# Kernel tuning notes

Measured on AMD Instinct MI355X. Metric: run time of the kernel, lower is better.

Reference implementation:

```python
import jax, jax.numpy as jnp
import numpy as np

N_P, N_V, N_C, N_A = 8000, 3000, 1500, 6000
CLS = N_C
D = 128
E = 150000
N_TOT = N_P + N_V + N_C + N_A
LAMBDA1 = 1.0


def _cal_matrix(A):
    # row-normalize, leaving all-zero rows untouched (matches cal_matrix)
    d = jnp.sum(A, axis=1)
    safe = jnp.where(d > 0, d, 1.0)
    return jnp.where((d > 0)[:, None], A / safe[:, None], A)


def _linear(x, W, b):
    return x @ W.T + b


def _gru(x, h, Wih, Whh, bih, bhh):
    # torch.nn.GRUCell semantics; gate order r, z, n
    gi = x @ Wih.T + bih
    gh = h @ Whh.T + bhh
    ir, iz, inn = jnp.split(gi, 3, axis=1)
    hr, hz, hn = jnp.split(gh, 3, axis=1)
    r = jax.nn.sigmoid(ir + hr)
    z = jax.nn.sigmoid(iz + hz)
    n = jnp.tanh(inn + r * hn)
    return (1.0 - z) * n + z * h


def _ce_soft(pred, label):
    # torch CrossEntropyLoss with probabilistic targets; NOTE: pred is already
    # softmaxed in the original, so log_softmax is applied on top (faithful double softmax)
    return -jnp.mean(jnp.sum(label * jax.nn.log_softmax(pred, axis=1), axis=1))


def _fuse(e0, e1, W2, b2, W3, b3):
    # attention fusion: leaky_relu(., 0) == relu; softmax over the NODE axis (faithful)
    a = jnp.concatenate([_linear(e0, W2, b2), _linear(e1, W3, b3)], axis=0)  # [2N,1]
    alpha = jax.nn.softmax(jax.nn.relu(a).reshape(2, -1, 1), axis=1)
    return jax.nn.relu(jnp.sum(alpha * jnp.stack([e0, e1], axis=0), axis=0))


def _forward(feat_P, feat_V, feat_C, feat_A, W1, b1, W2, b2, W3, b3,
             L00W, L00b, L01W, L01b, L10W, L10b, L11W, L11b, L12W, L12b,
             g0_Wih, g0_Whh, g0_bih, g0_bhh, g1_Wih, g1_Whh, g1_bih, g1_bhh,
             rel_emb, adj00, adj01, adj10, adj11, adj12, clsA, clsP, clsV, u_s, u_d):
    # self embeddings via shared linear1
    self_P = _linear(feat_P, W1, b1)
    self_V = _linear(feat_V, W1, b1)
    self_C = _linear(feat_C, W1, b1)
    self_A = _linear(feat_A, W1, b1)
    loss_tcp = jnp.float32(0.0)
    # ---- meta-path 0: V -> P -> A (GRUCell 0) ----
    pred = jax.nn.softmax(_linear(feat_V, L00W, L00b), axis=1)        # [N_V, CLS]
    loss_tcp += _ce_soft(pred, clsV)
    tcp = jnp.sum(pred * clsV, axis=1, keepdims=True)                 # bmm([N,1,C],[N,C,1])
    h = adj00 @ (tcp * feat_V)                                        # [N_P, D]
    state_P0 = _gru(feat_P, h, g0_Wih, g0_Whh, g0_bih, g0_bhh)
    pred = jax.nn.softmax(_linear(state_P0, L01W, L01b), axis=1)
    loss_tcp += _ce_soft(pred, clsP)
    tcp = jnp.sum(pred * clsP, axis=1, keepdims=True)
    h = adj01 @ (tcp * state_P0)                                      # [N_A, D]
    state_A0 = _gru(feat_A, h, g0_Wih, g0_Whh, g0_bih, g0_bhh)
    # ---- meta-path 1: A -> P -> V -> C (GRUCell 1) ----
    pred = jax.nn.softmax(_linear(feat_A, L10W, L10b), axis=1)
    loss_tcp += _ce_soft(pred, clsA)
    tcp = jnp.sum(pred * clsA, axis=1, keepdims=True)
    h = adj10 @ (tcp * feat_A)                                        # [N_P, D]
    state_P1 = _gru(feat_P, h, g1_Wih, g1_Whh, g1_bih, g1_bhh)        # appended 3rd, unused by fusion
    pred = jax.nn.softmax(_linear(state_P1, L11W, L11b), axis=1)
    loss_tcp += _ce_soft(pred, clsP)
    tcp = jnp.sum(pred * clsP, axis=1, keepdims=True)
    h = adj11 @ (tcp * state_P1)                                      # [N_V, D]
    state_V1 = _gru(feat_V, h, g1_Wih, g1_Whh, g1_bih, g1_bhh)
    pred = jax.nn.softmax(_linear(state_V1, L12W, L12b), axis=1)
    loss_tcp += _ce_soft(pred, clsV)
    tcp = jnp.sum(pred * clsV, axis=1, keepdims=True)
    h = adj12 @ (tcp * state_V1)                                      # [N_C, D]
    state_C1 = _gru(feat_C, h, g1_Wih, g1_Whh, g1_bih, g1_bhh)
    # ---- attention fusion of (self_emb, first GRU state) per node type ----
    emb_P = _fuse(self_P, state_P0, W2, b2, W3, b3)
    emb_V = _fuse(self_V, state_V1, W2, b2, W3, b3)
    emb_C = _fuse(self_C, state_C1, W2, b2, W3, b3)
    emb_A = _fuse(self_A, state_A0, W2, b2, W3, b3)
    final_ent = jnp.concatenate([emb_P, emb_V, emb_C, emb_A], axis=0)  # order P,V,C,A
    # ---- link scoring ----
    lab_d = u_d[:, 2].astype(jnp.float32)
    lab_s = u_s[:, 2].astype(jnp.float32)
    M_r = rel_emb[u_d[:, 3]]
    inner_d = jnp.sum(M_r * jnp.tanh(final_ent[u_d[:, 0]] + final_ent[u_d[:, 1]]), axis=1)
    inner_s = jnp.sum(final_ent[u_s[:, 0]] * final_ent[u_s[:, 1]], axis=1)
    base = -jnp.sum(jax.nn.log_sigmoid(lab_d * inner_d)) - jnp.sum(jax.nn.log_sigmoid(lab_s * inner_s))
    # l2_loss_emb is 0 in the original; l2_loss is computed but never added to loss_emb
    loss = base + LAMBDA1 * loss_tcp
    return loss, final_ent, rel_emb


def setup_inputs():
    key = jax.random.key(0)
    ki = iter(jax.random.split(key, 48))
    def nk():
        return next(ki)
    def xav(o, i):  # xavier_normal_
        return jax.random.normal(nk(), (o, i), jnp.float32) * jnp.sqrt(2.0 / (o + i))
    def uni(shape):  # torch GRUCell default init
        k = 1.0 / float(np.sqrt(D))
        return jax.random.uniform(nk(), shape, jnp.float32, -k, k)
    def radj(o, i, p=0.003):  # raw binary adjacency
        return (jax.random.uniform(nk(), (o, i)) < p).astype(jnp.float32)

    feat_P = jax.random.normal(nk(), (N_P, D), jnp.float32)
    feat_V = jax.random.normal(nk(), (N_V, D), jnp.float32)
    feat_C = jax.random.normal(nk(), (N_C, D), jnp.float32)
    feat_A = jax.random.normal(nk(), (N_A, D), jnp.float32)
    A00 = radj(N_P, N_V); A01 = radj(N_A, N_P)
    A10 = radj(N_P, N_A); A11 = radj(N_V, N_P); A12 = radj(N_C, N_V)

    inp = dict(
        feat_P=feat_P, feat_V=feat_V, feat_C=feat_C, feat_A=feat_A,
        W1=xav(D, D), b1=jnp.zeros((D,), jnp.float32),
        W2=xav(1, D), b2=jnp.zeros((1,), jnp.float32),
        W3=xav(1, D), b3=jnp.zeros((1,), jnp.float32),
        L00W=xav(CLS, D), L00b=jnp.zeros((CLS,), jnp.float32),
        L01W=xav(CLS, D), L01b=jnp.zeros((CLS,), jnp.float32),
        L10W=xav(CLS, D), L10b=jnp.zeros((CLS,), jnp.float32),
        L11W=xav(CLS, D), L11b=jnp.zeros((CLS,), jnp.float32),
        L12W=xav(CLS, D), L12b=jnp.zeros((CLS,), jnp.float32),
        g0_Wih=uni((3 * D, D)), g0_Whh=uni((3 * D, D)), g0_bih=uni((3 * D,)), g0_bhh=uni((3 * D,)),
        g1_Wih=uni((3 * D, D)), g1_Whh=uni((3 * D, D)), g1_bih=uni((3 * D,)), g1_bhh=uni((3 * D,)),
        rel_emb=jax.random.normal(nk(), (12, D), jnp.float32),
        adj00=_cal_matrix(A00), adj01=_cal_matrix(A01),
        adj10=_cal_matrix(A10), adj11=_cal_matrix(A11), adj12=_cal_matrix(A12),
        clsA=_cal_matrix((A12 @ (A11 @ A10)).T),   # [N_A, CLS]
        clsP=_cal_matrix((A12 @ A11).T),           # [N_P, CLS]
        clsV=_cal_matrix(A12.T),                   # [N_V, CLS]
    )

    def edges(n_cols):
        i = jax.random.randint(nk(), (E,), 0, N_TOT)
        j = jax.random.randint(nk(), (E,), 0, N_TOT)
        lab = jax.random.randint(nk(), (E,), 0, 2) * 2 - 1  # labels in {-1,+1}
        cols = [i, j, lab]
        if n_cols == 4:
            cols.append(jax.random.randint(nk(), (E,), 0, 12))
        return jnp.stack(cols, axis=1)

    inp['u_s'] = edges(3)
    inp['u_d'] = edges(4)
    return inp


def reference(feat_P, feat_V, feat_C, feat_A, W1, b1, W2, b2, W3, b3,
              L00W, L00b, L01W, L01b, L10W, L10b, L11W, L11b, L12W, L12b,
              g0_Wih, g0_Whh, g0_bih, g0_bhh, g1_Wih, g1_Whh, g1_bih, g1_bhh,
              rel_emb, adj00, adj01, adj10, adj11, adj12, clsA, clsP, clsV, u_s, u_d):
    return _forward(feat_P, feat_V, feat_C, feat_A, W1, b1, W2, b2, W3, b3,
                    L00W, L00b, L01W, L01b, L10W, L10b, L11W, L11b, L12W, L12b,
                    g0_Wih, g0_Whh, g0_bih, g0_bhh, g1_Wih, g1_Whh, g1_bih, g1_bhh,
                    rel_emb, adj00, adj01, adj10, adj11, adj12, clsA, clsP, clsV, u_s, u_d)
```

## Files before the change

kernel.cpp:

```cpp
#include <hip/hip_runtime.h>
#include <cstdint>
#include <cstddef>

#define DEV_INLINE __device__ __forceinline__

typedef __attribute__((ext_vector_type(8))) short bf16x8;
typedef __attribute__((ext_vector_type(16))) float f32x16;
struct __align__(8) US4 { unsigned short u[4]; };

DEV_INLINE unsigned short f2bf(float x) {
  unsigned u = __float_as_uint(x);
  return (unsigned short)((u + 0x7FFFu + ((u >> 16) & 1u)) >> 16);
}
DEV_INLINE float bf2f(unsigned short u) { return __uint_as_float(((unsigned)u) << 16); }
DEV_INLINE float2 bfpair(unsigned v) {
  return make_float2(__uint_as_float(v << 16), __uint_as_float(v & 0xFFFF0000u));
}
DEV_INLINE float ftanh(float x) {
  float e = __expf(2.0f * x);
  return 1.0f - 2.0f / (e + 1.0f);
}
DEV_INLINE float softplus_neg(float x) {
  return (x >= 0.f) ? log1pf(__expf(-x)) : (-x + log1pf(__expf(x)));
}

struct CvtSeg { const float* src; unsigned short* dst; int n; int nblk; };
struct CvtArgs { CvtSeg seg[16]; int nseg; };

__global__ __launch_bounds__(256) void convert_bf16_many(CvtArgs args) {
  int b = blockIdx.x;
  int s = 0;
  while (s < args.nseg && b >= args.seg[s].nblk) { b -= args.seg[s].nblk; ++s; }
  if (s >= args.nseg) return;
  int base = b * 1024 + threadIdx.x * 4;
  if (base >= args.seg[s].n) return;
  float4 v = *reinterpret_cast<const float4*>(args.seg[s].src + base);
  US4 o;
  o.u[0] = f2bf(v.x); o.u[1] = f2bf(v.y); o.u[2] = f2bf(v.z); o.u[3] = f2bf(v.w);
  *reinterpret_cast<US4*>(args.seg[s].dst + base) = o;
}

struct GSeg { const unsigned short* X; const unsigned short* W; const float* bias;
              float* C; unsigned short* Cb; int N; int O; int blk0; int xblk; };
struct GSegs { GSeg s[8]; int nseg; };

__global__ __launch_bounds__(256) void gemm_bf16_gseg(GSegs gs) {
  __shared__ __align__(16) unsigned short Xs[128 * 128];
  __shared__ __align__(16) unsigned short Ws[64 * 128];
  int bx = blockIdx.x;
  int si = 0;
  while (si + 1 < gs.nseg && bx >= gs.s[si + 1].blk0) ++si;
  const GSeg& g = gs.s[si];
  int b = bx - g.blk0;
  int bm = (b % g.xblk) * 128;
  int bn = (b / g.xblk) * 64;
  const int tid = threadIdx.x;

#pragma unroll
  for (int i = 0; i < 8; ++i) {
    int s = tid + 256 * i;
    int row = s >> 4, c16 = s & 15;
    uint4 v = make_uint4(0, 0, 0, 0);
    int gr = bm + row;
    if (gr < g.N) v = *reinterpret_cast<const uint4*>(g.X + (size_t)gr * 128 + c16 * 8);
    *reinterpret_cast<uint4*>(&Xs[(row * 16 + (c16 ^ (row & 7))) * 8]) = v;
  }
#pragma unroll
  for (int i = 0; i < 4; ++i) {
    int s = tid + 256 * i;
    int row = s >> 4, c16 = s & 15;
    uint4 v = make_uint4(0, 0, 0, 0);
    int gw = bn + row;
    if (gw < g.O) v = *reinterpret_cast<const uint4*>(g.W + (size_t)gw * 128 + c16 * 8);
    *reinterpret_cast<uint4*>(&Ws[(row * 16 + (c16 ^ (row & 7))) * 8]) = v;
  }
  __syncthreads();

  const int wave = tid >> 6, lane = tid & 63;
  const int l31 = lane & 31, lhi = lane >> 5;

  f32x16 acc0, acc1;
#pragma unroll
  for (int i = 0; i < 16; ++i) { acc0[i] = 0.f; acc1[i] = 0.f; }
  const int ar = wave * 32 + l31;
#pragma unroll
  for (int ks = 0; ks < 8; ++ks) {
    int c16 = ks * 2 + lhi;
    bf16x8 a  = *reinterpret_cast<const bf16x8*>(&Xs[(ar * 16 + (c16 ^ (ar & 7))) * 8]);
    bf16x8 b0 = *reinterpret_cast<const bf16x8*>(&Ws[(l31 * 16 + (c16 ^ (l31 & 7))) * 8]);
    int br1 = 32 + l31;
    bf16x8 b1 = *reinterpret_cast<const bf16x8*>(&Ws[(br1 * 16 + (c16 ^ (br1 & 7))) * 8]);
    acc0 = __builtin_amdgcn_mfma_f32_32x32x16_bf16(a, b0, acc0, 0, 0, 0);
    acc1 = __builtin_amdgcn_mfma_f32_32x32x16_bf16(a, b1, acc1, 0, 0, 0);
  }

  if (g.Cb) {
#pragma unroll
    for (int reg = 0; reg < 16; ++reg) {
      int r = bm + wave * 32 + (reg & 3) + 8 * (reg >> 2) + 4 * lhi;
      if (r < g.N) {
        int c0 = bn + l31;
        if (c0 < g.O) g.Cb[(size_t)r * g.O + c0] = f2bf(acc0[reg] + g.bias[c0]);
        int c1 = bn + 32 + l31;
        if (c1 < g.O) g.Cb[(size_t)r * g.O + c1] = f2bf(acc1[reg] + g.bias[c1]);
      }
    }
  } else {
#pragma unroll
    for (int reg = 0; reg < 16; ++reg) {
      int r = bm + wave * 32 + (reg & 3) + 8 * (reg >> 2) + 4 * lhi;
      if (r < g.N) {
        int c0 = bn + l31;
        if (c0 < g.O) g.C[(size_t)r * g.O + c0] = acc0[reg] + g.bias[c0];
        int c1 = bn + 32 + l31;
        if (c1 < g.O) g.C[(size_t)r * g.O + c1] = acc1[reg] + g.bias[c1];
      }
    }
  }
}

DEV_INLINE void spmv_body_b(const float* __restrict__ A, const float* __restrict__ Xs,
                            unsigned short* __restrict__ Hb, int row, int K,
                            float (*red)[128])
{
  int tid = threadIdx.x, wave = tid >> 6, lane = tid & 63;
  const float4* Arow = reinterpret_cast<const float4*>(A + (size_t)row * K);
  int K4 = K >> 2;
  float acc0 = 0.f, acc1 = 0.f;
  int base = wave * 64;
  int q = base + lane;
  float4 a = (base < K4 && q < K4) ? Arow[q] : make_float4(0.f, 0.f, 0.f, 0.f);
  for (; base < K4; base += 256) {
    int nb = base + 256;
    int nq = nb + lane;
    float4 an = (nb < K4 && nq < K4) ? Arow[nq] : make_float4(0.f, 0.f, 0.f, 0.f);
#pragma unroll
    for (int c = 0; c < 4; ++c) {
      float av = (c == 0) ? a.x : (c == 1) ? a.y : (c == 2) ? a.z : a.w;
      unsigned long long mm = __ballot(av != 0.f);
      while (mm) {
        int b = __builtin_ctzll(mm);
        mm &= mm - 1;
        float v = __shfl(av, b);
        int jj = (base + b) * 4 + c;
        const float* xr = Xs + (size_t)jj * 128;
        acc0 += v * xr[lane];
        acc1 += v * xr[lane + 64];
      }
    }
    a = an;
  }
  red[wave][lane] = acc0;
  red[wave][lane + 64] = acc1;
  __syncthreads();
  if (wave == 0) {
    float r0 = red[0][lane] + red[1][lane] + red[2][lane] + red[3][lane];
    float r1 = red[0][lane + 64] + red[1][lane + 64] + red[2][lane + 64] + red[3][lane + 64];
    Hb[(size_t)row * 128 + lane] = f2bf(r0);
    Hb[(size_t)row * 128 + 64 + lane] = f2bf(r1);
  }
}

__global__ __launch_bounds__(256) void spmv_scan(
    const float* __restrict__ A, const float* __restrict__ Xs,
    unsigned short* __restrict__ Hb, int M, int K)
{
  __shared__ float red[4][128];
  spmv_body_b(A, Xs, Hb, blockIdx.x, K, red);
}

__global__ __launch_bounds__(256) void spmv_scan2(
    const float* __restrict__ A0, const float* __restrict__ X0,
    unsigned short* __restrict__ H0b, int M0, int K0,
    const float* __restrict__ A1, const float* __restrict__ X1,
    unsigned short* __restrict__ H1b, int K1)
{
  __shared__ float red[4][128];
  if ((int)blockIdx.x < M0) spmv_body_b(A0, X0, H0b, blockIdx.x, K0, red);
  else                      spmv_body_b(A1, X1, H1b, blockIdx.x - M0, K1, red);
}

DEV_INLINE void ghgru_body_b(
    const unsigned short* __restrict__ Hb, const unsigned short* __restrict__ Whhb,
    const float* __restrict__ bhh, const unsigned short* __restrict__ gi,
    float* __restrict__ out, unsigned short* __restrict__ outb,
    int M, int bm, unsigned short* As)
{
  const int tid = threadIdx.x;
#pragma unroll
  for (int i = 0; i < 2; ++i) {
    int s = tid + 256 * i;
    int row = s >> 4, c16 = s & 15;
    uint4 v = make_uint4(0, 0, 0, 0);
    int gr = bm + row;
    if (gr < M) v = *reinterpret_cast<const uint4*>(Hb + (size_t)gr * 128 + c16 * 8);
    *reinterpret_cast<uint4*>(&As[(row * 16 + (c16 ^ (row & 7))) * 8]) = v;
  }
  __syncthreads();

  const int wave = tid >> 6, lane = tid & 63;
  const int l31 = lane & 31, lhi = lane >> 5;
  const int d = wave * 32 + l31;

  f32x16 ar, az, an;
#pragma unroll
  for (int i = 0; i < 16; ++i) { ar[i] = 0.f; az[i] = 0.f; an[i] = 0.f; }

#pragma unroll
  for (int ks = 0; ks < 8; ++ks) {
    int c16 = ks * 2 + lhi;
    bf16x8 a = *reinterpret_cast<const bf16x8*>(&As[(l31 * 16 + (c16 ^ (l31 & 7))) * 8]);
    const unsigned short* wb = Whhb + (size_t)c16 * 8;
    bf16x8 br = *reinterpret_cast<const bf16x8*>(wb + (size_t)d * 128);
    bf16x8 bz = *reinterpret_cast<const bf16x8*>(wb + (size_t)(128 + d) * 128);
    bf16x8 bn = *reinterpret_cast<const bf16x8*>(wb + (size_t)(256 + d) * 128);
    ar = __builtin_amdgcn_mfma_f32_32x32x16_bf16(a, br, ar, 0, 0, 0);
    az = __builtin_amdgcn_mfma_f32_32x32x16_bf16(a, bz, az, 0, 0, 0);
    an = __builtin_amdgcn_mfma_f32_32x32x16_bf16(a, bn, an, 0, 0, 0);
  }

  const float b_r = bhh[d], b_z = bhh[128 + d], b_n = bhh[256 + d];
#pragma unroll
  for (int reg = 0; reg < 16; ++reg) {
    int rowl = (reg & 3) + 8 * (reg >> 2) + 4 * lhi;
    int r = bm + rowl;
    if (r < M) {
      const unsigned short* gir = gi + (size_t)r * 384;
      float rr = 1.f / (1.f + __expf(-(bf2f(gir[d]) + ar[reg] + b_r)));
      float zz = 1.f / (1.f + __expf(-(bf2f(gir[128 + d]) + az[reg] + b_z)));
      float nn = ftanh(bf2f(gir[256 + d]) + rr * (an[reg] + b_n));
      float h = bf2f(As[(rowl * 16 + ((d >> 3) ^ (rowl & 7))) * 8 + (d & 7)]);
      float o = (1.f - zz) * nn + zz * h;
      out[(size_t)r * 128 + d] = o;
      outb[(size_t)r * 128 + d] = f2bf(o);
    }
  }
}

__global__ __launch_bounds__(256) void gh_gru(
    const unsigned short* __restrict__ Hb, const unsigned short* __restrict__ Whhb,
    const float* __restrict__ bhh, const unsigned short* __restrict__ gi,
    float* __restrict__ out, unsigned short* __restrict__ outb, int M)
{
  __shared__ __align__(16) unsigned short As[32 * 128];
  ghgru_body_b(Hb, Whhb, bhh, gi, out, outb, M, blockIdx.x * 32, As);
}

__global__ __launch_bounds__(256) void gh_gru2(
    const unsigned short* Hb0, const unsigned short* Whh0, const float* bhh0,
    const unsigned short* gi0, float* out0, unsigned short* outb0, int M0, int nblk0,
    const unsigned short* Hb1, const unsigned short* Whh1, const float* bhh1,
    const unsigned short* gi1, float* out1, unsigned short* outb1, int M1)
{
  __shared__ __align__(16) unsigned short As[32 * 128];
  if ((int)blockIdx.x < nblk0)
    ghgru_body_b(Hb0, Whh0, bhh0, gi0, out0, outb0, M0, blockIdx.x * 32, As);
  else
    ghgru_body_b(Hb1, Whh1, bhh1, gi1, out1, outb1, M1, (blockIdx.x - nblk0) * 32, As);
}

DEV_INLINE void rowops_body_b(int lane, const unsigned* __restrict__ lrb,
                              const float2* __restrict__ cr2,
                              const float* __restrict__ srcrow,
                              float* __restrict__ scaledrow, float* __restrict__ cep)
{
  float2 e[12];
  float m = -3.4e38f;
#pragma unroll
  for (int k = 0; k < 12; ++k) {
    int idx = k * 64 + lane;
    if (idx < 750) {
      e[k] = bfpair(lrb[idx]);
      m = fmaxf(m, fmaxf(e[k].x, e[k].y));
    } else {
      e[k] = make_float2(-3.4e38f, -3.4e38f);
    }
  }
#pragma unroll
  for (int o = 1; o < 64; o <<= 1) m = fmaxf(m, __shfl_xor(m, o));
  float z = 0.f;
#pragma unroll
  for (int k = 0; k < 12; ++k) {
    e[k].x = __expf(e[k].x - m); e[k].y = __expf(e[k].y - m);
    z += e[k].x + e[k].y;
  }
#pragma unroll
  for (int o = 1; o < 64; o <<= 1) z += __shfl_xor(z, o);
  float invZ1 = 1.0f / z;
  float m2 = invZ1;
  float t = 0.f, ls = 0.f, z2 = 0.f;
#pragma unroll
  for (int k = 0; k < 12; ++k) {
    int idx = k * 64 + lane;
    if (idx < 750) {
      float2 c = cr2[idx];
      float px = e[k].x * invZ1, py = e[k].y * invZ1;
      t  += c.x * px + c.y * py;
      ls += c.x + c.y;
      z2 += __expf(px - m2) + __expf(py - m2);
    }
  }
#pragma unroll
  for (int o = 1; o < 64; o <<= 1) {
    t += __shfl_xor(t, o); ls += __shfl_xor(ls, o); z2 += __shfl_xor(z2, o);
  }
  if (lane == 0) *cep = t - ls * (m2 + logf(z2));
  scaledrow[lane]      = t * srcrow[lane];
  scaledrow[lane + 64] = t * srcrow[lane + 64];
}

__global__ __launch_bounds__(256) void rowops2b(
    const unsigned* lgA, const float* clsA_, const float* srcA, float* scA, float* ceA, int nA,
    const unsigned* lgB, const float* clsB_, const float* srcB, float* scB, float* ceB, int nB)
{
  int gw = (blockIdx.x * 256 + threadIdx.x) >> 6;
  if (gw >= nA + nB) return;
  int lane = threadIdx.x & 63;
  if (gw < nA) {
    rowops_body_b(lane, lgA + (size_t)gw * 750,
                  reinterpret_cast<const float2*>(clsA_ + (size_t)gw * 1500),
                  srcA + (size_t)gw * 128, scA + (size_t)gw * 128, ceA + gw);
  } else {
    int r = gw - nA;
    rowops_body_b(lane, lgB + (size_t)r * 750,
                  reinterpret_cast<const float2*>(clsB_ + (size_t)r * 1500),
                  srcB + (size_t)r * 128, scB + (size_t)r * 128, ceB + r);
  }
}

__global__ __launch_bounds__(256) void rowops1b(
    const unsigned* lg, const float* cls, const float* src, float* sc, float* ce, int n)
{
  int gw = (blockIdx.x * 256 + threadIdx.x) >> 6;
  if (gw >= n) return;
  int lane = threadIdx.x & 63;
  rowops_body_b(lane, lg + (size_t)gw * 750,
                reinterpret_cast<const float2*>(cls + (size_t)gw * 1500),
                src + (size_t)gw * 128, sc + (size_t)gw * 128, ce + gw);
}

__global__ __launch_bounds__(256) void fuse_scores_all(
    const float* __restrict__ e0, const float* __restrict__ e1,
    const float* __restrict__ W2, const float* __restrict__ b2,
    const float* __restrict__ W3, const float* __restrict__ b3,
    float* __restrict__ s0, float* __restrict__ s1)
{
  int lane = threadIdx.x & 63;
  int row = (blockIdx.x * 256 + threadIdx.x) >> 6;
  if (row >= 18500) return;
  float a0 = e0[(size_t)row * 128 + lane] * W2[lane] + e0[(size_t)row * 128 + 64 + lane] * W2[64 + lane];
  float a1 = e1[(size_t)row * 128 + lane] * W3[lane] + e1[(size_t)row * 128 + 64 + lane] * W3[64 + lane];
#pragma unroll
  for (int o = 32; o > 0; o >>= 1) { a0 += __shfl_down(a0, o); a1 += __shfl_down(a1, o); }
  if (lane == 0) {
    s0[row] = fmaxf(a0 + b2[0], 0.f);
    s1[row] = fmaxf(a1 + b3[0], 0.f);
  }
}

__global__ __launch_bounds__(1024) void denom4(
    const float* __restrict__ s0, const float* __restrict__ s1,
    float* __restrict__ den)
{
  __shared__ float red[1024];
  const int ns[4]   = {8000, 3000, 1500, 6000};
  const int offs[4] = {0, 8000, 11000, 12500};
  int b = blockIdx.x;
  int n = ns[b];
  const float* p0 = s0 + offs[b];
  const float* p1 = s1 + offs[b];
  int tid = threadIdx.x;
  float m = -3.4e38f;
  for (int i = tid; i < n; i += 1024) m = fmaxf(m, p0[i]);
  red[tid] = m; __syncthreads();
  for (int s = 512; s > 0; s >>= 1) { if (tid < s) red[tid] = fmaxf(red[tid], red[tid + s]); __syncthreads(); }
  float m0 = red[0]; __syncthreads();
  float z = 0.f;
  for (int i = tid; i < n; i += 1024) z += __expf(p0[i] - m0);
  red[tid] = z; __syncthreads();
  for (int s = 512; s > 0; s >>= 1) { if (tid < s) red[tid] += red[tid + s]; __syncthreads(); }
  float Z0 = red[0]; __syncthreads();
  m = -3.4e38f;
  for (int i = tid; i < n; i += 1024) m = fmaxf(m, p1[i]);
  red[tid] = m; __syncthreads();
  for (int s = 512; s > 0; s >>= 1) { if (tid < s) red[tid] = fmaxf(red[tid], red[tid + s]); __syncthreads(); }
  float m1 = red[0]; __syncthreads();
  z = 0.f;
  for (int i = tid; i < n; i += 1024) z += __expf(p1[i] - m1);
  red[tid] = z; __syncthreads();
  for (int s = 512; s > 0; s >>= 1) { if (tid < s) red[tid] += red[tid + s]; __syncthreads(); }
  if (tid == 0) { den[b * 4] = m0; den[b * 4 + 1] = Z0; den[b * 4 + 2] = m1; den[b * 4 + 3] = red[0]; }
}

__global__ __launch_bounds__(256) void fuse_emb_all(
    const float* __restrict__ e0, const float* __restrict__ e1,
    const float* __restrict__ s0, const float* __restrict__ s1,
    const float* __restrict__ den, const float* __restrict__ rel,
    float* __restrict__ fe, unsigned short* __restrict__ feb,
    float* __restrict__ rel_out)
{
  int t = blockIdx.x * 256 + threadIdx.x;
  const int tot2 = 18500 * 64;
  if (t < tot2) {
    int idx = t * 2;
    int row = idx >> 7;
    int e = (row < 8000) ? 0 : (row < 11000) ? 1 : (row < 12500) ? 2 : 3;
    float a0 = __expf(s0[row] - den[e * 4]) / den[e * 4 + 1];
    float a1 = __expf(s1[row] - den[e * 4 + 2]) / den[e * 4 + 3];
    float2 v0 = *reinterpret_cast<const float2*>(e0 + idx);
    float2 v1 = *reinterpret_cast<const float2*>(e1 + idx);
    float r0 = fmaxf(a0 * v0.x + a1 * v1.x, 0.f);
    float r1 = fmaxf(a0 * v0.y + a1 * v1.y, 0.f);
    *reinterpret_cast<float2*>(fe + idx) = make_float2(r0, r1);
    unsigned pb = (unsigned)f2bf(r0) | ((unsigned)f2bf(r1) << 16);
    *reinterpret_cast<unsigned*>(feb + idx) = pb;
  } else if (t < tot2 + 768) {
    int k = (t - tot2) * 2;
    *reinterpret_cast<float2*>(rel_out + k) = *reinterpret_cast<const float2*>(rel + k);
  }
}

__global__ __launch_bounds__(256) void edge_both(
    const int* __restrict__ ud, const int* __restrict__ us,
    const unsigned short* __restrict__ feb, const unsigned short* __restrict__ relb,
    float* __restrict__ partial, int En)
{
  const int tid = threadIdx.x;
  const int lane = tid & 63;
  const int l = lane & 31, h = lane >> 5;
  const int wid = tid >> 6;
  bool is_d = (blockIdx.x < 1024);
  int bb = is_d ? blockIdx.x : blockIdx.x - 1024;
  int e = (bb * 4 + wid) * 2 + h;
  const int ns = 1024 * 4 * 2;
  float acc = 0.f;
  if (is_d) {
    int4 ei = (e < En) ? *reinterpret_cast<const int4*>(ud + (size_t)e * 4)
                       : make_int4(0, 0, 0, 0);
    for (; e < En; e += ns) {
      int en = e + ns;
      int4 ein = (en < En) ? *reinterpret_cast<const int4*>(ud + (size_t)en * 4)
                           : make_int4(0, 0, 0, 0);
      uint2 a = reinterpret_cast<const uint2*>(feb + (size_t)ei.x * 128)[l];
      uint2 b = reinterpret_cast<const uint2*>(feb + (size_t)ei.y * 128)[l];
      uint2 r = reinterpret_cast<const uint2*>(relb + (size_t)ei.w * 128)[l];
      float2 a0 = bfpair(a.x), a1 = bfpair(a.y);
      float2 b0 = bfpair(b.x), b1 = bfpair(b.y);
      float2 r0 = bfpair(r.x), r1 = bfpair(r.y);
      float d = r0.x * ftanh(a0.x + b0.x) + r0.y * ftanh(a0.y + b0.y)
              + r1.x * ftanh(a1.x + b1.x) + r1.y * ftanh(a1.y + b1.y);
#pragma unroll
      for (int o = 1; o < 32; o <<= 1) d += __shfl_xor(d, o);
      if (l == 0) acc += softplus_neg((float)ei.z * d);
      ei = ein;
    }
  } else {
    int3 ei = make_int3(0, 0, 0);
    if (e < En) { ei.x = us[(size_t)e * 3]; ei.y = us[(size_t)e * 3 + 1]; ei.z = us[(size_t)e * 3 + 2]; }
    for (; e < En; e += ns) {
      int en = e + ns;
      int3 ein = make_int3(0, 0, 0);
      if (en < En) { ein.x = us[(size_t)en * 3]; ein.y = us[(size_t)en * 3 + 1]; ein.z = us[(size_t)en * 3 + 2]; }
      uint2 a = reinterpret_cast<const uint2*>(feb + (size_t)ei.x * 128)[l];
      uint2 b = reinterpret_cast<const uint2*>(feb + (size_t)ei.y * 128)[l];
      float2 a0 = bfpair(a.x), a1 = bfpair(a.y);
      float2 b0 = bfpair(b.x), b1 = bfpair(b.y);
      float d = a0.x * b0.x + a0.y * b0.y + a1.x * b1.x + a1.y * b1.y;
#pragma unroll
      for (int o = 1; o < 32; o <<= 1) d += __shfl_xor(d, o);
      if (l == 0) acc += softplus_neg((float)ei.z * d);
      ei = ein;
    }
  }
  __shared__ float red[8];
  if (l == 0) red[wid * 2 + h] = acc;
  __syncthreads();
  if (tid == 0) {
    float s = 0.f;
#pragma unroll
    for (int i = 0; i < 8; ++i) s += red[i];
    partial[blockIdx.x] = s;
  }
}

__global__ __launch_bounds__(1024) void final_reduce(
    const float* __restrict__ partial, const float* __restrict__ cebuf,
    float* __restrict__ out)
{
  __shared__ float red[1024];
  __shared__ float total;
  int tid = threadIdx.x;
  if (tid == 0) total = 0.f;
  __syncthreads();
  float a = partial[tid] + partial[tid + 1024];
  red[tid] = a; __syncthreads();
  for (int s = 512; s > 0; s >>= 1) { if (tid < s) red[tid] += red[tid + s]; __syncthreads(); }
  if (tid == 0) total += red[0];
  __syncthreads();
  const int ns[5] = {3000, 8000, 6000, 8000, 3000};
#pragma unroll
  for (int seg = 0; seg < 5; ++seg) {
    const float* v = cebuf + seg * 8000;
    float s = 0.f;
    for (int i = tid; i < ns[seg]; i += 1024) s += v[i];
    red[tid] = s; __syncthreads();
    for (int st = 512; st > 0; st >>= 1) { if (tid < st) red[tid] += red[tid + st]; __syncthreads(); }
    if (tid == 0) total -= red[0] / (float)ns[seg];
    __syncthreads();
  }
  if (tid == 0) out[0] = total;
}

extern "C" void kernel_launch(void* const* d_in, const int* in_sizes, int n_in,
                              void* d_out, int out_size, void* d_ws, size_t ws_size,
                              hipStream_t stream)
{
  const float* feat_P = (const float*)d_in[0];
  const float* feat_V = (const float*)d_in[1];
  const float* feat_C = (const float*)d_in[2];
  const float* feat_A = (const float*)d_in[3];
  const float* W1 = (const float*)d_in[4];
  const float* b1 = (const float*)d_in[5];
  const float* W2 = (const float*)d_in[6];
  const float* b2 = (const float*)d_in[7];
  const float* W3 = (const float*)d_in[8];
  const float* b3 = (const float*)d_in[9];
  const float* L00W = (const float*)d_in[10];
  const float* L00b = (const float*)d_in[11];
  const float* L01W = (const float*)d_in[12];
  const float* L01b = (const float*)d_in[13];
  const float* L10W = (const float*)d_in[14];
  const float* L10b = (const float*)d_in[15];
  const float* L11W = (const float*)d_in[16];
  const float* L11b = (const float*)d_in[17];
  const float* L12W = (const float*)d_in[18];
  const float* L12b = (const float*)d_in[19];
  const float* g0_Wih = (const float*)d_in[20];
  const float* g0_Whh = (const float*)d_in[21];
  const float* g0_bih = (const float*)d_in[22];
  const float* g0_bhh = (const float*)d_in[23];
  const float* g1_Wih = (const float*)d_in[24];
  const float* g1_Whh = (const float*)d_in[25];
  const float* g1_bih = (const float*)d_in[26];
  const float* g1_bhh = (const float*)d_in[27];
  const float* rel_emb = (const float*)d_in[28];
  const float* adj00 = (const float*)d_in[29];
  const float* adj01 = (const float*)d_in[30];
  const float* adj10 = (const float*)d_in[31];
  const float* adj11 = (const float*)d_in[32];
  const float* adj12 = (const float*)d_in[33];
  const float* clsA = (const float*)d_in[34];
  const float* clsP = (const float*)d_in[35];
  const float* clsV = (const float*)d_in[36];
  const int* u_s = (const int*)d_in[37];
  const int* u_d = (const int*)d_in[38];

  float* out = (float*)d_out;
  float* fe = out + 1;
  float* rel_out = out + 1 + 18500 * 128;

  float* ws = (float*)d_ws;
  size_t o = 0;
  auto alloc = [&](size_t n) { float* p = ws + o; o += n; return p; };
  float* selfb   = alloc((size_t)18500 * 128);
  float* stcat   = alloc((size_t)18500 * 128);
  float* stP1    = alloc((size_t)8000 * 128);
  float* scaled0 = alloc((size_t)3000 * 128);
  float* scaled1 = alloc((size_t)8000 * 128);
  float* scaled2 = alloc((size_t)6000 * 128);
  float* scaled3 = alloc((size_t)8000 * 128);
  float* scaled4 = alloc((size_t)3000 * 128);
  float* cebuf   = alloc(5 * 8000);
  float* s0b = alloc(18500);
  float* s1b = alloc(18500);
  float* den = alloc(16);
  float* partial = alloc(2048);
  auto allocb = [&](size_t nelem) { unsigned short* p = (unsigned short*)(ws + o); o += (nelem + 1) / 2; return p; };
  unsigned short* featb  = allocb((size_t)18500 * 128);
  unsigned short* stcatb = allocb((size_t)18500 * 128);
  unsigned short* stP1b  = allocb((size_t)8000 * 128);
  unsigned short* feb    = allocb((size_t)18500 * 128);
  unsigned short* h0b    = allocb((size_t)8000 * 128);
  unsigned short* h2b    = allocb((size_t)8000 * 128);
  unsigned short* h1b    = allocb((size_t)6000 * 128);
  unsigned short* h3b    = allocb((size_t)3000 * 128);
  unsigned short* h4b    = allocb((size_t)1500 * 128);
  unsigned short* gib    = allocb((size_t)26500 * 384);
  unsigned short* lg0b   = allocb((size_t)3000 * 1500);
  unsigned short* lg2b   = allocb((size_t)6000 * 1500);
  unsigned short* lg1b   = allocb((size_t)8000 * 1500);
  unsigned short* lg3b   = allocb((size_t)8000 * 1500);
  unsigned short* relb   = allocb(12 * 128);
  unsigned short* W1b = allocb(128 * 128);
  unsigned short* L00Wb = allocb(1500 * 128);
  unsigned short* L01Wb = allocb(1500 * 128);
  unsigned short* L10Wb = allocb(1500 * 128);
  unsigned short* L11Wb = allocb(1500 * 128);
  unsigned short* L12Wb = allocb(1500 * 128);
  unsigned short* g0Wihb = allocb(384 * 128);
  unsigned short* g0Whhb = allocb(384 * 128);
  unsigned short* g1Wihb = allocb(384 * 128);
  unsigned short* g1Whhb = allocb(384 * 128);
  unsigned short* featPb = featb;
  unsigned short* featVb = featb + (size_t)8000 * 128;
  unsigned short* featCb = featb + (size_t)11000 * 128;
  unsigned short* featAb = featb + (size_t)12500 * 128;
  float* stP0 = stcat;
  float* stV1 = stcat + (size_t)8000 * 128;
  float* stC1 = stcat + (size_t)11000 * 128;
  float* stA0 = stcat + (size_t)12500 * 128;
  unsigned short* stP0b = stcatb;
  unsigned short* stV1b = stcatb + (size_t)8000 * 128;
  unsigned short* stC1b = stcatb + (size_t)11000 * 128;
  unsigned short* stA0b = stcatb + (size_t)12500 * 128;
  (void)ws_size; (void)in_sizes; (void)n_in; (void)out_size;

  dim3 blk(256);
  const size_t giOff[5] = {0, 8000, 14000, 22000, 25000};

  CvtArgs ca{};
  int nseg = 0, totblk = 0;
  auto addseg = [&](const float* src, unsigned short* dst, int n) {
    ca.seg[nseg].src = src; ca.seg[nseg].dst = dst; ca.seg[nseg].n = n;
    ca.seg[nseg].nblk = (n + 1023) / 1024; totblk += ca.seg[nseg].nblk; ++nseg;
  };
  addseg(feat_P, featPb, 8000 * 128);
  addseg(feat_V, featVb, 3000 * 128);
  addseg(feat_C, featCb, 1500 * 128);
  addseg(feat_A, featAb, 6000 * 128);
  addseg(W1, W1b, 128 * 128);
  addseg(L00W, L00Wb, 1500 * 128);
  addseg(L01W, L01Wb, 1500 * 128);
  addseg(L10W, L10Wb, 1500 * 128);
  addseg(L11W, L11Wb, 1500 * 128);
  addseg(L12W, L12Wb, 1500 * 128);
  addseg(g0_Wih, g0Wihb, 384 * 128);
  addseg(g0_Whh, g0Whhb, 384 * 128);
  addseg(g1_Wih, g1Wihb, 384 * 128);
  addseg(g1_Whh, g1Whhb, 384 * 128);
  addseg(rel_emb, relb, 12 * 128);
  ca.nseg = nseg;
  hipLaunchKernelGGL(convert_bf16_many, dim3(totblk), blk, 0, stream, ca);

  {
    GSegs gs{};
    int nb = 0, k = 0;
    auto add = [&](const unsigned short* X, const unsigned short* W, const float* bias,
                   float* C, unsigned short* Cb, int N, int O) {
      int xb = (N + 127) / 128, yb = (O + 63) / 64;
      gs.s[k] = GSeg{X, W, bias, C, Cb, N, O, nb, xb};
      nb += xb * yb; ++k;
    };
    add(featb,  W1b,    b1,     selfb, nullptr,                18500, 128);
    add(featPb, g0Wihb, g0_bih, nullptr, gib + giOff[0] * 384, 8000, 384);
    add(featAb, g0Wihb, g0_bih, nullptr, gib + giOff[1] * 384, 6000, 384);
    add(featPb, g1Wihb, g1_bih, nullptr, gib + giOff[2] * 384, 8000, 384);
    add(featVb, g1Wihb, g1_bih, nullptr, gib + giOff[3] * 384, 3000, 384);
    add(featCb, g1Wihb, g1_bih, nullptr, gib + giOff[4] * 384, 1500, 384);
    add(featVb, L00Wb,  L00b,   nullptr, lg0b,                 3000, 1500);
    add(featAb, L10Wb,  L10b,   nullptr, lg2b,                 6000, 1500);
    gs.nseg = k;
    hipLaunchKernelGGL(gemm_bf16_gseg, dim3(nb), blk, 0, stream, gs);
  }

  hipLaunchKernelGGL(rowops2b, dim3((9000 * 64 + 255) / 256), blk, 0, stream,
                     (const unsigned*)lg0b, clsV, feat_V, scaled0, cebuf + 0 * 8000, 3000,
                     (const unsigned*)lg2b, clsA, feat_A, scaled2, cebuf + 2 * 8000, 6000);
  hipLaunchKernelGGL(spmv_scan2, dim3(16000), blk, 0, stream,
                     adj00, scaled0, h0b, 8000, 3000,
                     adj10, scaled2, h2b, 6000);
  hipLaunchKernelGGL(gh_gru2, dim3(500), blk, 0, stream,
                     h0b, g0Whhb, g0_bhh, gib + giOff[0] * 384, stP0, stP0b, 8000, 250,
                     h2b, g1Whhb, g1_bhh, gib + giOff[2] * 384, stP1, stP1b, 8000);
  {
    GSegs gs{};
    gs.s[0] = GSeg{stP0b, L01Wb, L01b, nullptr, lg1b, 8000, 1500, 0,    63};
    gs.s[1] = GSeg{stP1b, L11Wb, L11b, nullptr, lg3b, 8000, 1500, 1512, 63};
    gs.nseg = 2;
    hipLaunchKernelGGL(gemm_bf16_gseg, dim3(3024), blk, 0, stream, gs);
  }
  hipLaunchKernelGGL(rowops2b, dim3((16000 * 64 + 255) / 256), blk, 0, stream,
                     (const unsigned*)lg1b, clsP, stP0, scaled1, cebuf + 1 * 8000, 8000,
                     (const unsigned*)lg3b, clsP, stP1, scaled3, cebuf + 3 * 8000, 8000);
  hipLaunchKernelGGL(spmv_scan2, dim3(9000), blk, 0, stream,
                     adj01, scaled1, h1b, 6000, 8000,
                     adj11, scaled3, h3b, 8000);
  hipLaunchKernelGGL(gh_gru2, dim3(188 + 94), blk, 0, stream,
                     h1b, g0Whhb, g0_bhh, gib + giOff[1] * 384, stA0, stA0b, 6000, 188,
                     h3b, g1Whhb, g1_bhh, gib + giOff[3] * 384, stV1, stV1b, 3000);
  {
    GSegs gs{};
    gs.s[0] = GSeg{stV1b, L12Wb, L12b, nullptr, lg1b, 3000, 1500, 0, 24};
    gs.nseg = 1;
    hipLaunchKernelGGL(gemm_bf16_gseg, dim3(24 * 24), blk, 0, stream, gs);
  }
  hipLaunchKernelGGL(rowops1b, dim3((3000 * 64 + 255) / 256), blk, 0, stream,
                     (const unsigned*)lg1b, clsV, stV1, scaled4, cebuf + 4 * 8000, 3000);
  hipLaunchKernelGGL(spmv_scan, dim3(1500), blk, 0, stream, adj12, scaled4, h4b, 1500, 3000);
  hipLaunchKernelGGL(gh_gru, dim3(47), blk, 0, stream,
                     h4b, g1Whhb, g1_bhh, gib + giOff[4] * 384, stC1, stC1b, 1500);

  hipLaunchKernelGGL(fuse_scores_all, dim3((18500 + 3) / 4), blk, 0, stream,
                     selfb, stcat, W2, b2, W3, b3, s0b, s1b);
  hipLaunchKernelGGL(denom4, dim3(4), dim3(1024), 0, stream, s0b, s1b, den);
  hipLaunchKernelGGL(fuse_emb_all, dim3((18500 * 64 + 768 + 255) / 256), blk, 0, stream,
                     selfb, stcat, s0b, s1b, den, rel_emb, fe, feb, rel_out);

  hipLaunchKernelGGL(edge_both, dim3(2048), blk, 0, stream, u_d, u_s, feb, relb, partial, 150000);

  hipLaunchKernelGGL(final_reduce, dim3(1), dim3(1024), 0, stream, partial, cebuf, out);
}
```

Baseline: 495.8 us.

## Keep intermediate embeddings in bf16 only, fuse paired rowops, prefetch edge gathers

Drops the fp32 copies of the GRU states and self embeddings, so the GEMM and GRU kernels write only bf16 and downstream rowops and fusion kernels read bf16 pairs. This roughly halves the bytes written and read for these tensors. The two rowops over P that share clsP are merged into one kernel that reads the class matrix once. The edge loss loop now issues the next edge's feature gathers before computing the current one, to hide memory latency. In exchange, the rowops scaling and the fusion inputs now use bf16-rounded values, which slightly lowers precision.

```diff
diff --git a/kernel.cpp b/kernel.cpp
--- a/kernel.cpp
+++ b/kernel.cpp
@@ -183,8 +183,7 @@
 DEV_INLINE void ghgru_body_b(
     const unsigned short* __restrict__ Hb, const unsigned short* __restrict__ Whhb,
     const float* __restrict__ bhh, const unsigned short* __restrict__ gi,
-    float* __restrict__ out, unsigned short* __restrict__ outb,
-    int M, int bm, unsigned short* As)
+    unsigned short* __restrict__ outb, int M, int bm, unsigned short* As)
 {
   const int tid = threadIdx.x;
 #pragma unroll
@@ -231,7 +230,6 @@
       float nn = ftanh(bf2f(gir[256 + d]) + rr * (an[reg] + b_n));
       float h = bf2f(As[(rowl * 16 + ((d >> 3) ^ (rowl & 7))) * 8 + (d & 7)]);
       float o = (1.f - zz) * nn + zz * h;
-      out[(size_t)r * 128 + d] = o;
       outb[(size_t)r * 128 + d] = f2bf(o);
     }
   }
@@ -240,28 +238,28 @@
 __global__ __launch_bounds__(256) void gh_gru(
     const unsigned short* __restrict__ Hb, const unsigned short* __restrict__ Whhb,
     const float* __restrict__ bhh, const unsigned short* __restrict__ gi,
-    float* __restrict__ out, unsigned short* __restrict__ outb, int M)
+    unsigned short* __restrict__ outb, int M)
 {
   __shared__ __align__(16) unsigned short As[32 * 128];
-  ghgru_body_b(Hb, Whhb, bhh, gi, out, outb, M, blockIdx.x * 32, As);
+  ghgru_body_b(Hb, Whhb, bhh, gi, outb, M, blockIdx.x * 32, As);
 }
 
 __global__ __launch_bounds__(256) void gh_gru2(
     const unsigned short* Hb0, const unsigned short* Whh0, const float* bhh0,
-    const unsigned short* gi0, float* out0, unsigned short* outb0, int M0, int nblk0,
+    const unsigned short* gi0, unsigned short* outb0, int M0, int nblk0,
     const unsigned short* Hb1, const unsigned short* Whh1, const float* bhh1,
-    const unsigned short* gi1, float* out1, unsigned short* outb1, int M1)
+    const unsigned short* gi1, unsigned short* outb1, int M1)
 {
   __shared__ __align__(16) unsigned short As[32 * 128];
   if ((int)blockIdx.x < nblk0)
-    ghgru_body_b(Hb0, Whh0, bhh0, gi0, out0, outb0, M0, blockIdx.x * 32, As);
+    ghgru_body_b(Hb0, Whh0, bhh0, gi0, outb0, M0, blockIdx.x * 32, As);
   else
-    ghgru_body_b(Hb1, Whh1, bhh1, gi1, out1, outb1, M1, (blockIdx.x - nblk0) * 32, As);
+    ghgru_body_b(Hb1, Whh1, bhh1, gi1, outb1, M1, (blockIdx.x - nblk0) * 32, As);
 }
 
 DEV_INLINE void rowops_body_b(int lane, const unsigned* __restrict__ lrb,
                               const float2* __restrict__ cr2,
-                              const float* __restrict__ srcrow,
+                              const unsigned* __restrict__ srcb,
                               float* __restrict__ scaledrow, float* __restrict__ cep)
 {
   float2 e[12];
@@ -305,13 +303,13 @@
     t += __shfl_xor(t, o); ls += __shfl_xor(ls, o); z2 += __shfl_xor(z2, o);
   }
   if (lane == 0) *cep = t - ls * (m2 + logf(z2));
-  scaledrow[lane]      = t * srcrow[lane];
-  scaledrow[lane + 64] = t * srcrow[lane + 64];
+  float2 sv = bfpair(srcb[lane]);
+  *reinterpret_cast<float2*>(scaledrow + lane * 2) = make_float2(t * sv.x, t * sv.y);
 }
 
 __global__ __launch_bounds__(256) void rowops2b(
-    const unsigned* lgA, const float* clsA_, const float* srcA, float* scA, float* ceA, int nA,
-    const unsigned* lgB, const float* clsB_, const float* srcB, float* scB, float* ceB, int nB)
+    const unsigned* lgA, const float* clsA_, const unsigned* srcA, float* scA, float* ceA, int nA,
+    const unsigned* lgB, const float* clsB_, const unsigned* srcB, float* scB, float* ceB, int nB)
 {
   int gw = (blockIdx.x * 256 + threadIdx.x) >> 6;
   if (gw >= nA + nB) return;
@@ -319,28 +317,102 @@
   if (gw < nA) {
     rowops_body_b(lane, lgA + (size_t)gw * 750,
                   reinterpret_cast<const float2*>(clsA_ + (size_t)gw * 1500),
-                  srcA + (size_t)gw * 128, scA + (size_t)gw * 128, ceA + gw);
+                  srcA + (size_t)gw * 64, scA + (size_t)gw * 128, ceA + gw);
   } else {
     int r = gw - nA;
     rowops_body_b(lane, lgB + (size_t)r * 750,
                   reinterpret_cast<const float2*>(clsB_ + (size_t)r * 1500),
-                  srcB + (size_t)r * 128, scB + (size_t)r * 128, ceB + r);
+                  srcB + (size_t)r * 64, scB + (size_t)r * 128, ceB + r);
   }
 }
 
 __global__ __launch_bounds__(256) void rowops1b(
-    const unsigned* lg, const float* cls, const float* src, float* sc, float* ce, int n)
+    const unsigned* lg, const float* cls, const unsigned* src, float* sc, float* ce, int n)
 {
   int gw = (blockIdx.x * 256 + threadIdx.x) >> 6;
   if (gw >= n) return;
   int lane = threadIdx.x & 63;
   rowops_body_b(lane, lg + (size_t)gw * 750,
                 reinterpret_cast<const float2*>(cls + (size_t)gw * 1500),
-                src + (size_t)gw * 128, sc + (size_t)gw * 128, ce + gw);
+                src + (size_t)gw * 64, sc + (size_t)gw * 128, ce + gw);
+}
+
+__global__ __launch_bounds__(256) void rowops_pairb(
+    const unsigned* lg1, const unsigned* lg3, const float* clsP,
+    const unsigned* src1, const unsigned* src3,
+    float* sc1, float* sc3, float* ce1, float* ce3, int n)
+{
+  int gw = (blockIdx.x * 256 + threadIdx.x) >> 6;
+  if (gw >= n) return;
+  int lane = threadIdx.x & 63;
+  const unsigned* l1 = lg1 + (size_t)gw * 750;
+  const unsigned* l3 = lg3 + (size_t)gw * 750;
+  const float2* cr2 = reinterpret_cast<const float2*>(clsP + (size_t)gw * 1500);
+
+  float2 e1[12], e3[12];
+  float m1 = -3.4e38f, m3 = -3.4e38f;
+#pragma unroll
+  for (int k = 0; k < 12; ++k) {
+    int idx = k * 64 + lane;
+    if (idx < 750) {
+      e1[k] = bfpair(l1[idx]);
+      e3[k] = bfpair(l3[idx]);
+      m1 = fmaxf(m1, fmaxf(e1[k].x, e1[k].y));
+      m3 = fmaxf(m3, fmaxf(e3[k].x, e3[k].y));
+    } else {
+      e1[k] = make_float2(-3.4e38f, -3.4e38f);
+      e3[k] = make_float2(-3.4e38f, -3.4e38f);
+    }
+  }
+#pragma unroll
+  for (int o = 1; o < 64; o <<= 1) {
+    m1 = fmaxf(m1, __shfl_xor(m1, o));
+    m3 = fmaxf(m3, __shfl_xor(m3, o));
+  }
+  float z1 = 0.f, z3 = 0.f;
+#pragma unroll
+  for (int k = 0; k < 12; ++k) {
+    e1[k].x = __expf(e1[k].x - m1); e1[k].y = __expf(e1[k].y - m1);
+    e3[k].x = __expf(e3[k].x - m3); e3[k].y = __expf(e3[k].y - m3);
+    z1 += e1[k].x + e1[k].y;
+    z3 += e3[k].x + e3[k].y;
+  }
+#pragma unroll
+  for (int o = 1; o < 64; o <<= 1) { z1 += __shfl_xor(z1, o); z3 += __shfl_xor(z3, o); }
+  float iZ1 = 1.0f / z1, iZ3 = 1.0f / z3;
+  float q1 = iZ1, q3 = iZ3;
+  float t1 = 0.f, t3 = 0.f, ls = 0.f, w1 = 0.f, w3 = 0.f;
+#pragma unroll
+  for (int k = 0; k < 12; ++k) {
+    int idx = k * 64 + lane;
+    if (idx < 750) {
+      float2 c = cr2[idx];
+      float p1x = e1[k].x * iZ1, p1y = e1[k].y * iZ1;
+      float p3x = e3[k].x * iZ3, p3y = e3[k].y * iZ3;
+      t1 += c.x * p1x + c.y * p1y;
+      t3 += c.x * p3x + c.y * p3y;
+      ls += c.x + c.y;
+      w1 += __expf(p1x - q1) + __expf(p1y - q1);
+      w3 += __expf(p3x - q3) + __expf(p3y - q3);
+    }
+  }
+#pragma unroll
+  for (int o = 1; o < 64; o <<= 1) {
+    t1 += __shfl_xor(t1, o); t3 += __shfl_xor(t3, o); ls += __shfl_xor(ls, o);
+    w1 += __shfl_xor(w1, o); w3 += __shfl_xor(w3, o);
+  }
+  if (lane == 0) {
+    ce1[gw] = t1 - ls * (q1 + logf(w1));
+    ce3[gw] = t3 - ls * (q3 + logf(w3));
+  }
+  float2 s1 = bfpair(src1[(size_t)gw * 64 + lane]);
+  float2 s3 = bfpair(src3[(size_t)gw * 64 + lane]);
+  *reinterpret_cast<float2*>(sc1 + (size_t)gw * 128 + lane * 2) = make_float2(t1 * s1.x, t1 * s1.y);
+  *reinterpret_cast<float2*>(sc3 + (size_t)gw * 128 + lane * 2) = make_float2(t3 * s3.x, t3 * s3.y);
 }
 
 __global__ __launch_bounds__(256) void fuse_scores_all(
-    const float* __restrict__ e0, const float* __restrict__ e1,
+    const unsigned* __restrict__ e0, const unsigned* __restrict__ e1,
     const float* __restrict__ W2, const float* __restrict__ b2,
     const float* __restrict__ W3, const float* __restrict__ b3,
     float* __restrict__ s0, float* __restrict__ s1)
@@ -348,8 +420,12 @@
   int lane = threadIdx.x & 63;
   int row = (blockIdx.x * 256 + threadIdx.x) >> 6;
   if (row >= 18500) return;
-  float a0 = e0[(size_t)row * 128 + lane] * W2[lane] + e0[(size_t)row * 128 + 64 + lane] * W2[64 + lane];
-  float a1 = e1[(size_t)row * 128 + lane] * W3[lane] + e1[(size_t)row * 128 + 64 + lane] * W3[64 + lane];
+  float2 w2 = *reinterpret_cast<const float2*>(W2 + lane * 2);
+  float2 w3 = *reinterpret_cast<const float2*>(W3 + lane * 2);
+  float2 v0 = bfpair(e0[(size_t)row * 64 + lane]);
+  float2 v1 = bfpair(e1[(size_t)row * 64 + lane]);
+  float a0 = v0.x * w2.x + v0.y * w2.y;
+  float a1 = v1.x * w3.x + v1.y * w3.y;
 #pragma unroll
   for (int o = 32; o > 0; o >>= 1) { a0 += __shfl_down(a0, o); a1 += __shfl_down(a1, o); }
   if (lane == 0) {
@@ -393,7 +469,7 @@
 }
 
 __global__ __launch_bounds__(256) void fuse_emb_all(
-    const float* __restrict__ e0, const float* __restrict__ e1,
+    const unsigned* __restrict__ e0, const unsigned* __restrict__ e1,
     const float* __restrict__ s0, const float* __restrict__ s1,
     const float* __restrict__ den, const float* __restrict__ rel,
     float* __restrict__ fe, unsigned short* __restrict__ feb,
@@ -407,8 +483,8 @@
     int e = (row < 8000) ? 0 : (row < 11000) ? 1 : (row < 12500) ? 2 : 3;
     float a0 = __expf(s0[row] - den[e * 4]) / den[e * 4 + 1];
     float a1 = __expf(s1[row] - den[e * 4 + 2]) / den[e * 4 + 3];
-    float2 v0 = *reinterpret_cast<const float2*>(e0 + idx);
-    float2 v1 = *reinterpret_cast<const float2*>(e1 + idx);
+    float2 v0 = bfpair(e0[t]);
+    float2 v1 = bfpair(e1[t]);
     float r0 = fmaxf(a0 * v0.x + a1 * v1.x, 0.f);
     float r1 = fmaxf(a0 * v0.y + a1 * v1.y, 0.f);
     *reinterpret_cast<float2*>(fe + idx) = make_float2(r0, r1);
@@ -437,39 +513,44 @@
   if (is_d) {
     int4 ei = (e < En) ? *reinterpret_cast<const int4*>(ud + (size_t)e * 4)
                        : make_int4(0, 0, 0, 0);
+    uint2 av = reinterpret_cast<const uint2*>(feb + (size_t)ei.x * 128)[l];
+    uint2 bv = reinterpret_cast<const uint2*>(feb + (size_t)ei.y * 128)[l];
+    uint2 rv = reinterpret_cast<const uint2*>(relb + (size_t)ei.w * 128)[l];
     for (; e < En; e += ns) {
       int en = e + ns;
       int4 ein = (en < En) ? *reinterpret_cast<const int4*>(ud + (size_t)en * 4)
                            : make_int4(0, 0, 0, 0);
-      uint2 a = reinterpret_cast<const uint2*>(feb + (size_t)ei.x * 128)[l];
-      uint2 b = reinterpret_cast<const uint2*>(feb + (size_t)ei.y * 128)[l];
-      uint2 r = reinterpret_cast<const uint2*>(relb + (size_t)ei.w * 128)[l];
-      float2 a0 = bfpair(a.x), a1 = bfpair(a.y);
-      float2 b0 = bfpair(b.x), b1 = bfpair(b.y);
-      float2 r0 = bfpair(r.x), r1 = bfpair(r.y);
+      uint2 avn = reinterpret_cast<const uint2*>(feb + (size_t)ein.x * 128)[l];
+      uint2 bvn = reinterpret_cast<const uint2*>(feb + (size_t)ein.y * 128)[l];
+      uint2 rvn = reinterpret_cast<const uint2*>(relb + (size_t)ein.w * 128)[l];
+      float2 a0 = bfpair(av.x), a1 = bfpair(av.y);
+      float2 b0 = bfpair(bv.x), b1 = bfpair(bv.y);
+      float2 r0 = bfpair(rv.x), r1 = bfpair(rv.y);
       float d = r0.x * ftanh(a0.x + b0.x) + r0.y * ftanh(a0.y + b0.y)
               + r1.x * ftanh(a1.x + b1.x) + r1.y * ftanh(a1.y + b1.y);
 #pragma unroll
       for (int o = 1; o < 32; o <<= 1) d += __shfl_xor(d, o);
       if (l == 0) acc += softplus_neg((float)ei.z * d);
-      ei = ein;
+      ei = ein; av = avn; bv = bvn; rv = rvn;
     }
   } else {
     int3 ei = make_int3(0, 0, 0);
     if (e < En) { ei.x = us[(size_t)e * 3]; ei.y = us[(size_t)e * 3 + 1]; ei.z = us[(size_t)e * 3 + 2]; }
+    uint2 av = reinterpret_cast<const uint2*>(feb + (size_t)ei.x * 128)[l];
+    uint2 bv = reinterpret_cast<const uint2*>(feb + (size_t)ei.y * 128)[l];
     for (; e < En; e += ns) {
       int en = e + ns;
       int3 ein = make_int3(0, 0, 0);
       if (en < En) { ein.x = us[(size_t)en * 3]; ein.y = us[(size_t)en * 3 + 1]; ein.z = us[(size_t)en * 3 + 2]; }
-      uint2 a = reinterpret_cast<const uint2*>(feb + (size_t)ei.x * 128)[l];
-      uint2 b = reinterpret_cast<const uint2*>(feb + (size_t)ei.y * 128)[l];
-      float2 a0 = bfpair(a.x), a1 = bfpair(a.y);
-      float2 b0 = bfpair(b.x), b1 = bfpair(b.y);
+      uint2 avn = reinterpret_cast<const uint2*>(feb + (size_t)ein.x * 128)[l];
+      uint2 bvn = reinterpret_cast<const uint2*>(feb + (size_t)ein.y * 128)[l];
+      float2 a0 = bfpair(av.x), a1 = bfpair(av.y);
+      float2 b0 = bfpair(bv.x), b1 = bfpair(bv.y);
       float d = a0.x * b0.x + a0.y * b0.y + a1.x * b1.x + a1.y * b1.y;
 #pragma unroll
       for (int o = 1; o < 32; o <<= 1) d += __shfl_xor(d, o);
       if (l == 0) acc += softplus_neg((float)ei.z * d);
-      ei = ein;
+      ei = ein; av = avn; bv = bvn;
     }
   }
   __shared__ float red[8];
@@ -562,9 +643,6 @@
   float* ws = (float*)d_ws;
   size_t o = 0;
   auto alloc = [&](size_t n) { float* p = ws + o; o += n; return p; };
-  float* selfb   = alloc((size_t)18500 * 128);
-  float* stcat   = alloc((size_t)18500 * 128);
-  float* stP1    = alloc((size_t)8000 * 128);
   float* scaled0 = alloc((size_t)3000 * 128);
   float* scaled1 = alloc((size_t)8000 * 128);
   float* scaled2 = alloc((size_t)6000 * 128);
@@ -577,6 +655,7 @@
   float* partial = alloc(2048);
   auto allocb = [&](size_t nelem) { unsigned short* p = (unsigned short*)(ws + o); o += (nelem + 1) / 2; return p; };
   unsigned short* featb  = allocb((size_t)18500 * 128);
+  unsigned short* selfbB = allocb((size_t)18500 * 128);
   unsigned short* stcatb = allocb((size_t)18500 * 128);
   unsigned short* stP1b  = allocb((size_t)8000 * 128);
   unsigned short* feb    = allocb((size_t)18500 * 128);
@@ -605,10 +684,6 @@
   unsigned short* featVb = featb + (size_t)8000 * 128;
   unsigned short* featCb = featb + (size_t)11000 * 128;
   unsigned short* featAb = featb + (size_t)12500 * 128;
-  float* stP0 = stcat;
-  float* stV1 = stcat + (size_t)8000 * 128;
-  float* stC1 = stcat + (size_t)11000 * 128;
-  float* stA0 = stcat + (size_t)12500 * 128;
   unsigned short* stP0b = stcatb;
   unsigned short* stV1b = stcatb + (size_t)8000 * 128;
   unsigned short* stC1b = stcatb + (size_t)11000 * 128;
@@ -646,32 +721,32 @@
     GSegs gs{};
     int nb = 0, k = 0;
     auto add = [&](const unsigned short* X, const unsigned short* W, const float* bias,
-                   float* C, unsigned short* Cb, int N, int O) {
+                   unsigned short* Cb, int N, int O) {
       int xb = (N + 127) / 128, yb = (O + 63) / 64;
-      gs.s[k] = GSeg{X, W, bias, C, Cb, N, O, nb, xb};
+      gs.s[k] = GSeg{X, W, bias, nullptr, Cb, N, O, nb, xb};
       nb += xb * yb; ++k;
     };
-    add(featb,  W1b,    b1,     selfb, nullptr,                18500, 128);
-    add(featPb, g0Wihb, g0_bih, nullptr, gib + giOff[0] * 384, 8000, 384);
-    add(featAb, g0Wihb, g0_bih, nullptr, gib + giOff[1] * 384, 6000, 384);
-    add(featPb, g1Wihb, g1_bih, nullptr, gib + giOff[2] * 384, 8000, 384);
-    add(featVb, g1Wihb, g1_bih, nullptr, gib + giOff[3] * 384, 3000, 384);
-    add(featCb, g1Wihb, g1_bih, nullptr, gib + giOff[4] * 384, 1500, 384);
-    add(featVb, L00Wb,  L00b,   nullptr, lg0b,                 3000, 1500);
-    add(featAb, L10Wb,  L10b,   nullptr, lg2b,                 6000, 1500);
+    add(featb,  W1b,    b1,     selfbB,               18500, 128);
+    add(featPb, g0Wihb, g0_bih, gib + giOff[0] * 384, 8000, 384);
+    add(featAb, g0Wihb, g0_bih, gib + giOff[1] * 384, 6000, 384);
+    add(featPb, g1Wihb, g1_bih, gib + giOff[2] * 384, 8000, 384);
+    add(featVb, g1Wihb, g1_bih, gib + giOff[3] * 384, 3000, 384);
+    add(featCb, g1Wihb, g1_bih, gib + giOff[4] * 384, 1500, 384);
+    add(featVb, L00Wb,  L00b,   lg0b,                 3000, 1500);
+    add(featAb, L10Wb,  L10b,   lg2b,                 6000, 1500);
     gs.nseg = k;
     hipLaunchKernelGGL(gemm_bf16_gseg, dim3(nb), blk, 0, stream, gs);
   }
 
   hipLaunchKernelGGL(rowops2b, dim3((9000 * 64 + 255) / 256), blk, 0, stream,
-                     (const unsigned*)lg0b, clsV, feat_V, scaled0, cebuf + 0 * 8000, 3000,
-                     (const unsigned*)lg2b, clsA, feat_A, scaled2, cebuf + 2 * 8000, 6000);
+                     (const unsigned*)lg0b, clsV, (const unsigned*)featVb, scaled0, cebuf + 0 * 8000, 3000,
+                     (const unsigned*)lg2b, clsA, (const unsigned*)featAb, scaled2, cebuf + 2 * 8000, 6000);
   hipLaunchKernelGGL(spmv_scan2, dim3(16000), blk, 0, stream,
                      adj00, scaled0, h0b, 8000, 3000,
                      adj10, scaled2, h2b, 6000);
   hipLaunchKernelGGL(gh_gru2, dim3(500), blk, 0, stream,
-                     h0b, g0Whhb, g0_bhh, gib + giOff[0] * 384, stP0, stP0b, 8000, 250,
-                     h2b, g1Whhb, g1_bhh, gib + giOff[2] * 384, stP1, stP1b, 8000);
+                     h0b, g0Whhb, g0_bhh, gib + giOff[0] * 384, stP0b, 8000, 250,
+                     h2b, g1Whhb, g1_bhh, gib + giOff[2] * 384, stP1b, 8000);
   {
     GSegs gs{};
     gs.s[0] = GSeg{stP0b, L01Wb, L01b, nullptr, lg1b, 8000, 1500, 0,    63};
@@ -679,15 +754,16 @@
     gs.nseg = 2;
     hipLaunchKernelGGL(gemm_bf16_gseg, dim3(3024), blk, 0, stream, gs);
   }
-  hipLaunchKernelGGL(rowops2b, dim3((16000 * 64 + 255) / 256), blk, 0, stream,
-                     (const unsigned*)lg1b, clsP, stP0, scaled1, cebuf + 1 * 8000, 8000,
-                     (const unsigned*)lg3b, clsP, stP1, scaled3, cebuf + 3 * 8000, 8000);
+  hipLaunchKernelGGL(rowops_pairb, dim3((8000 * 64 + 255) / 256), blk, 0, stream,
+                     (const unsigned*)lg1b, (const unsigned*)lg3b, clsP,
+                     (const unsigned*)stP0b, (const unsigned*)stP1b,
+                     scaled1, scaled3, cebuf + 1 * 8000, cebuf + 3 * 8000, 8000);
   hipLaunchKernelGGL(spmv_scan2, dim3(9000), blk, 0, stream,
                      adj01, scaled1, h1b, 6000, 8000,
                      adj11, scaled3, h3b, 8000);
   hipLaunchKernelGGL(gh_gru2, dim3(188 + 94), blk, 0, stream,
-                     h1b, g0Whhb, g0_bhh, gib + giOff[1] * 384, stA0, stA0b, 6000, 188,
-                     h3b, g1Whhb, g1_bhh, gib + giOff[3] * 384, stV1, stV1b, 3000);
+                     h1b, g0Whhb, g0_bhh, gib + giOff[1] * 384, stA0b, 6000, 188,
+                     h3b, g1Whhb, g1_bhh, gib + giOff[3] * 384, stV1b, 3000);
   {
     GSegs gs{};
     gs.s[0] = GSeg{stV1b, L12Wb, L12b, nullptr, lg1b, 3000, 1500, 0, 24};
@@ -695,16 +771,17 @@
     hipLaunchKernelGGL(gemm_bf16_gseg, dim3(24 * 24), blk, 0, stream, gs);
   }
   hipLaunchKernelGGL(rowops1b, dim3((3000 * 64 + 255) / 256), blk, 0, stream,
-                     (const unsigned*)lg1b, clsV, stV1, scaled4, cebuf + 4 * 8000, 3000);
+                     (const unsigned*)lg1b, clsV, (const unsigned*)stV1b,
+                     scaled4, cebuf + 4 * 8000, 3000);
   hipLaunchKernelGGL(spmv_scan, dim3(1500), blk, 0, stream, adj12, scaled4, h4b, 1500, 3000);
   hipLaunchKernelGGL(gh_gru, dim3(47), blk, 0, stream,
-                     h4b, g1Whhb, g1_bhh, gib + giOff[4] * 384, stC1, stC1b, 1500);
+                     h4b, g1Whhb, g1_bhh, gib + giOff[4] * 384, stC1b, 1500);
 
   hipLaunchKernelGGL(fuse_scores_all, dim3((18500 + 3) / 4), blk, 0, stream,
-                     selfb, stcat, W2, b2, W3, b3, s0b, s1b);
+                     (const unsigned*)selfbB, (const unsigned*)stcatb, W2, b2, W3, b3, s0b, s1b);
   hipLaunchKernelGGL(denom4, dim3(4), dim3(1024), 0, stream, s0b, s1b, den);
   hipLaunchKernelGGL(fuse_emb_all, dim3((18500 * 64 + 768 + 255) / 256), blk, 0, stream,
-                     selfb, stcat, s0b, s1b, den, rel_emb, fe, feb, rel_out);
+                     (const unsigned*)selfbB, (const unsigned*)stcatb, s0b, s1b, den, rel_emb, fe, feb, rel_out);
 
   hipLaunchKernelGGL(edge_both, dim3(2048), blk, 0, stream, u_d, u_s, feb, relb, partial, 150000);
 
```

New measurement: 490.2 us. About the same (-1.1%).
